# Optimization experiments

Measured on AMD Instinct MI355X. Metric: run time of the kernel, lower is better.

The kernel has to match this reference:

```python
import jax, jax.numpy as jnp
import numpy as np

B, S, D, H = 16, 512, 256, 8
DH = D // H


def setup_inputs() -> dict:
    key = jax.random.key(0)
    ks = jax.random.split(key, 10)
    w_scale = 1.0 / np.sqrt(D)
    query = jax.random.normal(ks[0], (B, S, D), dtype=jnp.float32)
    key_t = jax.random.normal(ks[1], (B, S, D), dtype=jnp.float32)
    value = jax.random.normal(ks[2], (B, S, D), dtype=jnp.float32)
    rel = jax.random.uniform(ks[3], (B, S, S), dtype=jnp.float32)
    timestamp = jax.random.uniform(ks[4], (B, S, S), dtype=jnp.float32) * 100.0
    # causal mask: True = masked (future), as used by masked_fill in the torch code
    mask = jnp.broadcast_to(jnp.triu(jnp.ones((S, S), dtype=bool), k=1), (B, S, S))
    l1 = jnp.array(0.3, dtype=jnp.float32)
    l2 = jnp.array(0.4, dtype=jnp.float32)
    Wq = jax.random.normal(ks[5], (D, D), dtype=jnp.float32) * w_scale
    Wk = jax.random.normal(ks[6], (D, D), dtype=jnp.float32) * w_scale
    Wv = jax.random.normal(ks[7], (D, D), dtype=jnp.float32) * w_scale
    bq = jnp.zeros((D,), dtype=jnp.float32)
    bk = jnp.zeros((D,), dtype=jnp.float32)
    bv = jnp.zeros((D,), dtype=jnp.float32)
    return {"query": query, "key": key_t, "value": value, "rel": rel,
            "timestamp": timestamp, "mask": mask, "l1": l1, "l2": l2,
            "Wq": Wq, "bq": bq, "Wk": Wk, "bk": bk, "Wv": Wv, "bv": bv}


def _proj(x, W, b):
    # nn.Linear: x @ W.T + b, then split heads -> [B, H, S, DH]
    return (x @ W.T + b).reshape(B, S, H, DH).transpose(0, 2, 1, 3)


def reference(query, key, value, rel, timestamp, mask, l1, l2,
              Wq, bq, Wk, bk, Wv, bv):
    q = _proj(query, Wq, bq)
    k = _proj(key, Wk, bk)
    v = _proj(value, Wv, bv)
    m = mask[:, None]                      # [B,1,S,S], broadcasts over heads
    # relative-coefficient attention: keep rel where mask True, -10000 elsewhere
    relf = rel[:, None] * m.astype(jnp.float32)
    rel_attn = jax.nn.softmax(jnp.where(relf == 0, jnp.float32(-10000.0), relf), axis=-1)
    # scaled dot-product scores
    scores = jnp.einsum('bhqd,bhkd->bhqk', q, k) / jnp.sqrt(jnp.float32(DH))
    scores = jnp.where(m, jnp.float32(-1e9), scores)
    # time-decay attention
    ts = jnp.exp(-jnp.abs(timestamp))[:, None]
    ts = jnp.where(m, -jnp.inf, ts)
    prob_attn = jax.nn.softmax(scores, axis=-1)
    time_attn = jax.nn.softmax(ts, axis=-1)
    prob_attn = (1 - l2) * prob_attn + l2 * time_attn
    prob_attn = (1 - l1) * prob_attn + l1 * rel_attn
    out = jnp.einsum('bhqk,bhkd->bhqd', prob_attn, v)
    out = out.transpose(0, 2, 1, 3).reshape(B, S, D)
    return out, prob_attn
```

## Files before the change

kernel.cpp:

```cpp
#include <hip/hip_runtime.h>
#include <hip/hip_bf16.h>

static constexpr int cB  = 16;
static constexpr int cS  = 512;
static constexpr int cD  = 256;
static constexpr int cH  = 8;
static constexpr int cDH = 32;
static constexpr size_t cNE = (size_t)cB * cS * cD;

typedef __attribute__((ext_vector_type(8))) short short8v;
typedef __attribute__((ext_vector_type(4))) short short4v;
typedef __attribute__((ext_vector_type(4))) float f32x4;

__device__ __forceinline__ short bfbits(float x) {
    __hip_bfloat16 h = __float2bfloat16(x);
    short s; __builtin_memcpy(&s, &h, 2); return s;
}
__device__ __forceinline__ float bff(short s) {
    __hip_bfloat16 h; __builtin_memcpy(&h, &s, 2); return __bfloat162float(h);
}

__global__ __launch_bounds__(256) void proj_kernel(
    const float* __restrict__ q_in, const float* __restrict__ k_in,
    const float* __restrict__ v_in,
    const float* __restrict__ Wq, const float* __restrict__ bq,
    const float* __restrict__ Wk, const float* __restrict__ bk,
    const float* __restrict__ Wv, const float* __restrict__ bv,
    float* __restrict__ ws)
{
    const int z = blockIdx.y;
    const float* X    = (z == 0) ? q_in : (z == 1) ? k_in : v_in;
    const float* W    = (z == 0) ? Wq   : (z == 1) ? Wk   : Wv;
    const float* bias = (z == 0) ? bq   : (z == 1) ? bk   : bv;
    short* HI  = (short*)ws + (size_t)z * 2 * cNE;
    short* LO  = HI + cNE;
    short* VTb = (short*)(ws + 2 * cNE);

    const int tid  = threadIdx.x;
    const int w    = tid >> 6;
    const int lane = tid & 63;
    const int n16  = lane & 15;
    const int quad = lane >> 4;

    const int i0 = blockIdx.x * 32 + 16 * (w & 1);
    const int j0 = 128 * (w >> 1);

    const float* xrow = X + (size_t)(i0 + n16) * cD + quad * 8;
    short8v a_hi[8], a_lo[8];
#pragma unroll
    for (int c = 0; c < 8; c++) {
        float xa[8];
        *(float4*)&xa[0] = *(const float4*)(xrow + c * 32);
        *(float4*)&xa[4] = *(const float4*)(xrow + c * 32 + 4);
#pragma unroll
        for (int j = 0; j < 8; j++) {
            short hb = bfbits(xa[j]);
            a_hi[c][j] = hb;
            a_lo[c][j] = bfbits(xa[j] - bff(hb));
        }
    }

#pragma unroll
    for (int t = 0; t < 8; t++) {
        const int jb = j0 + t * 16;
        const float* wrow = W + (size_t)(jb + n16) * cD + quad * 8;
        f32x4 acc = (f32x4){0.f, 0.f, 0.f, 0.f};
#pragma unroll
        for (int c = 0; c < 8; c++) {
            float wv_[8];
            *(float4*)&wv_[0] = *(const float4*)(wrow + c * 32);
            *(float4*)&wv_[4] = *(const float4*)(wrow + c * 32 + 4);
            short8v b_hi, b_lo;
#pragma unroll
            for (int j = 0; j < 8; j++) {
                short hb = bfbits(wv_[j]);
                b_hi[j] = hb;
                b_lo[j] = bfbits(wv_[j] - bff(hb));
            }
            acc = __builtin_amdgcn_mfma_f32_16x16x32_bf16(a_hi[c], b_hi, acc, 0, 0, 0);
            acc = __builtin_amdgcn_mfma_f32_16x16x32_bf16(a_hi[c], b_lo, acc, 0, 0, 0);
            acc = __builtin_amdgcn_mfma_f32_16x16x32_bf16(a_lo[c], b_hi, acc, 0, 0, 0);
        }
        const int jg = jb + n16;
        const float bv_ = bias[jg];
        const int h_ = jg >> 5, dh = jg & 31;
        if (z == 2) {
#pragma unroll
            for (int r = 0; r < 4; r++) {
                int gi = i0 + quad * 4 + r;
                int b_ = gi >> 9, s_ = gi & 511;
                VTb[(((size_t)(b_ * cH + h_)) * cDH + dh) * cS + s_] =
                    bfbits(acc[r] + bv_);
            }
        } else {
#pragma unroll
            for (int r = 0; r < 4; r++) {
                int gi = i0 + quad * 4 + r;
                int b_ = gi >> 9, s_ = gi & 511;
                size_t idx = (((size_t)(b_ * cH + h_)) * cS + s_) * cDH + dh;
                float v = acc[r] + bv_;
                short hb2 = bfbits(v);
                HI[idx] = hb2;
                LO[idx] = bfbits(v - bff(hb2));
            }
        }
    }
}

__global__ __launch_bounds__(256) void ev_kernel(
    const float* __restrict__ rel, const float* __restrict__ ts,
    const float* __restrict__ l1p, const float* __restrict__ l2p,
    short* __restrict__ Evb)
{
    const int w = threadIdx.x >> 6, lane = threadIdx.x & 63;
    const int row = blockIdx.x * 4 + w;
    const int q = row & 511;
    const float* tr = ts  + (size_t)row * cS;
    const float* rr = rel + (size_t)row * cS;
    const float l1 = l1p[0], l2 = l2p[0];
    const float Bc = (1.f - l1) * l2;
    const float Cc = l1;

    float tv[8], rv[8];
    float tmax = -1e30f, rmax = -1e30f;
#pragma unroll
    for (int j = 0; j < 8; j++) {
        int k = lane + 64 * j;
        float tl_ = (k <= q) ? tr[k] : 0.f;
        float r   = (k >  q) ? rr[k] : 0.f;
        tv[j] = (k <= q) ? __expf(-fabsf(tl_)) : -1e30f;
        rv[j] = (k > q && r != 0.f) ? r : -10000.f;
        tmax = fmaxf(tmax, tv[j]);
        rmax = fmaxf(rmax, rv[j]);
    }
#pragma unroll
    for (int m = 1; m < 64; m <<= 1) {
        tmax = fmaxf(tmax, __shfl_xor(tmax, m, 64));
        rmax = fmaxf(rmax, __shfl_xor(rmax, m, 64));
    }
    float te[8], re[8];
    float tsum = 0.f, rsum = 0.f;
#pragma unroll
    for (int j = 0; j < 8; j++) {
        te[j] = (tv[j] > -1e29f) ? __expf(tv[j] - tmax) : 0.f;
        re[j] = __expf(rv[j] - rmax);
        tsum += te[j]; rsum += re[j];
    }
#pragma unroll
    for (int m = 1; m < 64; m <<= 1) {
        tsum += __shfl_xor(tsum, m, 64);
        rsum += __shfl_xor(rsum, m, 64);
    }
    const float ti = Bc / tsum, ri = Cc / rsum;
#pragma unroll
    for (int j = 0; j < 8; j++) {
        int k = lane + 64 * j;
        Evb[(size_t)row * cS + k] = bfbits(te[j] * ti + re[j] * ri);
    }
}

__global__ __launch_bounds__(256, 4) void attn2_kernel(
    const float* __restrict__ ws, const short* __restrict__ Evb,
    const float* __restrict__ l1p, const float* __restrict__ l2p,
    float* __restrict__ out, float* __restrict__ prob)
{
    constexpr int PS = 536;
    __shared__ short Pl[32 * PS];
    __shared__ float redM[2][32];
    __shared__ float redS[2][32];

    const int tid  = threadIdx.x;
    const int w    = tid >> 6;
    const int lane = tid & 63;
    const int n16  = lane & 15;
    const int quad = lane >> 4;

    const int flat = blockIdx.y * gridDim.x + blockIdx.x;
    const int xcd  = flat & 7;
    const int slot = flat >> 3;
    const int b  = xcd + 8 * (slot >> 7);
    const int h  = (slot >> 4) & 7;
    const int qt = slot & 15;
    const size_t bh = (size_t)b * cH + h;
    const int q0 = qt * 32;

    const short* Qhi = (const short*)ws;
    const short* Qlo = Qhi + cNE;
    const short* Khi = Qhi + 2 * cNE;
    const short* Klo = Qhi + 3 * cNE;
    const short* VTb = (const short*)(ws + 2 * cNE);

    const float l1 = l1p[0], l2 = l2p[0];
    const float Ac = (1.f - l1) * (1.f - l2);

    const int qhH = w & 1;
    const int kh2 = w >> 1;
    const int kbase = 256 * kh2;

    const int rowA = q0 + 16 * qhH + n16;
    const size_t qoff = (bh * cS + rowA) * cDH + quad * 8;
    short8v a_hi = *(const short8v*)(Qhi + qoff);
    short8v a_lo = *(const short8v*)(Qlo + qoff);

    const int tl = (kbase <= q0 + 31) ? min(15, (q0 + 31 - kbase) >> 4) : -1;
    f32x4 acc[16];
#pragma unroll
    for (int t = 0; t < 16; t++) {
        acc[t] = (f32x4){0.f, 0.f, 0.f, 0.f};
        if (t <= tl) {
            const size_t koff = (bh * cS + kbase + 16 * t + n16) * cDH + quad * 8;
            short8v b_hi = *(const short8v*)(Khi + koff);
            short8v b_lo = *(const short8v*)(Klo + koff);
            acc[t] = __builtin_amdgcn_mfma_f32_16x16x32_bf16(a_hi, b_hi, acc[t], 0, 0, 0);
            acc[t] = __builtin_amdgcn_mfma_f32_16x16x32_bf16(a_hi, b_lo, acc[t], 0, 0, 0);
            acc[t] = __builtin_amdgcn_mfma_f32_16x16x32_bf16(a_lo, b_hi, acc[t], 0, 0, 0);
        }
    }

    const float scale = 0.17677669529663687f;
    const int rowDl = 16 * qhH + quad * 4;
    float Mx0 = -1e30f, Mx1 = -1e30f, Mx2 = -1e30f, Mx3 = -1e30f;
#pragma unroll
    for (int t = 0; t < 16; t++) {
        const int kg = kbase + 16 * t + n16;
        const int rg = q0 + rowDl;
        float s0 = (kg <= rg + 0) ? acc[t][0] * scale : -1e30f;
        float s1 = (kg <= rg + 1) ? acc[t][1] * scale : -1e30f;
        float s2 = (kg <= rg + 2) ? acc[t][2] * scale : -1e30f;
        float s3 = (kg <= rg + 3) ? acc[t][3] * scale : -1e30f;
        acc[t][0] = s0; acc[t][1] = s1; acc[t][2] = s2; acc[t][3] = s3;
        Mx0 = fmaxf(Mx0, s0); Mx1 = fmaxf(Mx1, s1);
        Mx2 = fmaxf(Mx2, s2); Mx3 = fmaxf(Mx3, s3);
    }
#pragma unroll
    for (int m = 1; m < 16; m <<= 1) {
        Mx0 = fmaxf(Mx0, __shfl_xor(Mx0, m, 64));
        Mx1 = fmaxf(Mx1, __shfl_xor(Mx1, m, 64));
        Mx2 = fmaxf(Mx2, __shfl_xor(Mx2, m, 64));
        Mx3 = fmaxf(Mx3, __shfl_xor(Mx3, m, 64));
    }
    if (n16 == 0) {
        redM[kh2][rowDl + 0] = Mx0; redM[kh2][rowDl + 1] = Mx1;
        redM[kh2][rowDl + 2] = Mx2; redM[kh2][rowDl + 3] = Mx3;
    }
    __syncthreads();
    float Mg0 = fmaxf(redM[0][rowDl + 0], redM[1][rowDl + 0]);
    float Mg1 = fmaxf(redM[0][rowDl + 1], redM[1][rowDl + 1]);
    float Mg2 = fmaxf(redM[0][rowDl + 2], redM[1][rowDl + 2]);
    float Mg3 = fmaxf(redM[0][rowDl + 3], redM[1][rowDl + 3]);

    float S0 = 0.f, S1 = 0.f, S2 = 0.f, S3 = 0.f;
#pragma unroll
    for (int t = 0; t < 16; t++) {
        float e0 = __expf(acc[t][0] - Mg0);
        float e1 = __expf(acc[t][1] - Mg1);
        float e2 = __expf(acc[t][2] - Mg2);
        float e3 = __expf(acc[t][3] - Mg3);
        acc[t][0] = e0; acc[t][1] = e1; acc[t][2] = e2; acc[t][3] = e3;
        S0 += e0; S1 += e1; S2 += e2; S3 += e3;
    }
#pragma unroll
    for (int m = 1; m < 16; m <<= 1) {
        S0 += __shfl_xor(S0, m, 64); S1 += __shfl_xor(S1, m, 64);
        S2 += __shfl_xor(S2, m, 64); S3 += __shfl_xor(S3, m, 64);
    }
    if (n16 == 0) {
        redS[kh2][rowDl + 0] = S0; redS[kh2][rowDl + 1] = S1;
        redS[kh2][rowDl + 2] = S2; redS[kh2][rowDl + 3] = S3;
    }
    __syncthreads();
    const float i0 = Ac / (redS[0][rowDl + 0] + redS[1][rowDl + 0]);
    const float i1 = Ac / (redS[0][rowDl + 1] + redS[1][rowDl + 1]);
    const float i2 = Ac / (redS[0][rowDl + 2] + redS[1][rowDl + 2]);
    const float i3 = Ac / (redS[0][rowDl + 3] + redS[1][rowDl + 3]);

#pragma unroll
    for (int t = 0; t < 16; t++) {
        const int col = kbase + 16 * t + n16;
        Pl[(rowDl + 0) * PS + col] = bfbits(acc[t][0] * i0);
        Pl[(rowDl + 1) * PS + col] = bfbits(acc[t][1] * i1);
        Pl[(rowDl + 2) * PS + col] = bfbits(acc[t][2] * i2);
        Pl[(rowDl + 3) * PS + col] = bfbits(acc[t][3] * i3);
    }
    __syncthreads();

#pragma unroll
    for (int it = 0; it < 16; it++) {
        const int idx = it * 256 + tid;
        const int r = idx >> 7;
        const int c0 = (idx & 127) * 4;
        short* pp = &Pl[r * PS + c0];
        short4v pv = *(short4v*)pp;
        const short4v ev = *(const short4v*)(Evb + ((size_t)(b * cS + q0 + r)) * cS + c0);
        f32x4 o;
#pragma unroll
        for (int j = 0; j < 4; j++) o[j] = bff(pv[j]) + bff(ev[j]);
        __builtin_nontemporal_store(o, (f32x4*)(prob + (bh * cS + q0 + r) * cS + c0));
#pragma unroll
        for (int j = 0; j < 4; j++) pv[j] = bfbits(o[j]);
        *(short4v*)pp = pv;
    }
    __syncthreads();

    const int dhT = w & 1, qT = w >> 1;
    const int dhA = 16 * dhT + n16;
    const short* vtrow = VTb + (bh * cDH + dhA) * cS;
    f32x4 oacc = (f32x4){0.f, 0.f, 0.f, 0.f};
#pragma unroll
    for (int k0 = 0; k0 < cS; k0 += 32) {
        short8v av = *(const short8v*)(vtrow + k0 + quad * 8);
        short8v bv = *(short8v*)&Pl[(16 * qT + n16) * PS + k0 + quad * 8];
        oacc = __builtin_amdgcn_mfma_f32_16x16x32_bf16(av, bv, oacc, 0, 0, 0);
    }
    const int qg = q0 + 16 * qT + n16;
    const int dhD = 16 * dhT + quad * 4;
    float* op = out + ((size_t)b * cS + qg) * cD + h * cDH + dhD;
    __builtin_nontemporal_store(oacc, (f32x4*)op);
}

extern "C" void kernel_launch(void* const* d_in, const int* in_sizes, int n_in,
                              void* d_out, int out_size, void* d_ws, size_t ws_size,
                              hipStream_t stream) {
    const float* query = (const float*)d_in[0];
    const float* key   = (const float*)d_in[1];
    const float* value = (const float*)d_in[2];
    const float* rel   = (const float*)d_in[3];
    const float* tsp   = (const float*)d_in[4];
    const float* l1 = (const float*)d_in[6];
    const float* l2 = (const float*)d_in[7];
    const float* Wq = (const float*)d_in[8];
    const float* bq = (const float*)d_in[9];
    const float* Wk = (const float*)d_in[10];
    const float* bk = (const float*)d_in[11];
    const float* Wv = (const float*)d_in[12];
    const float* bv = (const float*)d_in[13];

    float* ws   = (float*)d_ws;
    short* Evb  = (short*)(ws + 3 * cNE);
    float* out  = (float*)d_out;
    float* prob = out + cNE;

    proj_kernel<<<dim3(256, 3), 256, 0, stream>>>(query, key, value,
                                                  Wq, bq, Wk, bk, Wv, bv, ws);
    ev_kernel<<<dim3(2048), 256, 0, stream>>>(rel, tsp, l1, l2, Evb);
    attn2_kernel<<<dim3(16, 128), 256, 0, stream>>>(ws, Evb, l1, l2, out, prob);
}
```

Before: 289.4 us.

## Pre-split weights to bf16 hi/lo once and fuse projection with mixing-prep kernel

```diff
diff --git a/kernel.cpp b/kernel.cpp
--- a/kernel.cpp
+++ b/kernel.cpp
@@ -7,6 +7,7 @@
 static constexpr int cH  = 8;
 static constexpr int cDH = 32;
 static constexpr size_t cNE = (size_t)cB * cS * cD;
+static constexpr size_t cWN = (size_t)cD * cD;
 
 typedef __attribute__((ext_vector_type(8))) short short8v;
 typedef __attribute__((ext_vector_type(4))) short short4v;
@@ -20,142 +21,155 @@
     __hip_bfloat16 h; __builtin_memcpy(&h, &s, 2); return __bfloat162float(h);
 }
 
-__global__ __launch_bounds__(256) void proj_kernel(
-    const float* __restrict__ q_in, const float* __restrict__ k_in,
-    const float* __restrict__ v_in,
-    const float* __restrict__ Wq, const float* __restrict__ bq,
-    const float* __restrict__ Wk, const float* __restrict__ bk,
-    const float* __restrict__ Wv, const float* __restrict__ bv,
-    float* __restrict__ ws)
+__global__ __launch_bounds__(256) void wsplit_kernel(
+    const float* __restrict__ Wq, const float* __restrict__ Wk,
+    const float* __restrict__ Wv, short* __restrict__ Wsp)
 {
     const int z = blockIdx.y;
-    const float* X    = (z == 0) ? q_in : (z == 1) ? k_in : v_in;
-    const float* W    = (z == 0) ? Wq   : (z == 1) ? Wk   : Wv;
-    const float* bias = (z == 0) ? bq   : (z == 1) ? bk   : bv;
-    short* HI  = (short*)ws + (size_t)z * 2 * cNE;
-    short* LO  = HI + cNE;
-    short* VTb = (short*)(ws + 2 * cNE);
-
-    const int tid  = threadIdx.x;
+    const float* W = (z == 0) ? Wq : (z == 1) ? Wk : Wv;
+    short* hi = Wsp + (size_t)z * 2 * cWN;
+    short* lo = hi + cWN;
+    const int i = (blockIdx.x * 256 + threadIdx.x) * 4;
+    float4 v = *(const float4*)(W + i);
+    float va[4] = {v.x, v.y, v.z, v.w};
+    short4v h, l;
+#pragma unroll
+    for (int j = 0; j < 4; j++) {
+        short hb = bfbits(va[j]);
+        h[j] = hb;
+        l[j] = bfbits(va[j] - bff(hb));
+    }
+    *(short4v*)(hi + i) = h;
+    *(short4v*)(lo + i) = l;
+}
+
+__global__ __launch_bounds__(256) void prep_kernel(
+    const float* __restrict__ q_in, const float* __restrict__ k_in,
+    const float* __restrict__ v_in, const short* __restrict__ Wsp,
+    const float* __restrict__ bq, const float* __restrict__ bk,
+    const float* __restrict__ bv,
+    const float* __restrict__ rel, const float* __restrict__ ts,
+    const float* __restrict__ l1p, const float* __restrict__ l2p,
+    float* __restrict__ ws, short* __restrict__ Evb)
+{
+    const int bid = blockIdx.x;
+    const int tid = threadIdx.x;
     const int w    = tid >> 6;
     const int lane = tid & 63;
-    const int n16  = lane & 15;
-    const int quad = lane >> 4;
-
-    const int i0 = blockIdx.x * 32 + 16 * (w & 1);
-    const int j0 = 128 * (w >> 1);
-
-    const float* xrow = X + (size_t)(i0 + n16) * cD + quad * 8;
-    short8v a_hi[8], a_lo[8];
-#pragma unroll
-    for (int c = 0; c < 8; c++) {
-        float xa[8];
-        *(float4*)&xa[0] = *(const float4*)(xrow + c * 32);
-        *(float4*)&xa[4] = *(const float4*)(xrow + c * 32 + 4);
+
+    if (bid < 768) {
+        const int z  = bid >> 8;
+        const int bx = bid & 255;
+        const float* X    = (z == 0) ? q_in : (z == 1) ? k_in : v_in;
+        const float* bias = (z == 0) ? bq   : (z == 1) ? bk   : bv;
+        const short* Whi = Wsp + (size_t)z * 2 * cWN;
+        const short* Wlo = Whi + cWN;
+        short* HI  = (short*)ws + (size_t)z * 2 * cNE;
+        short* LO  = HI + cNE;
+        short* VTb = (short*)(ws + 2 * cNE);
+
+        const int n16  = lane & 15;
+        const int quad = lane >> 4;
+        const int i0 = bx * 32 + 16 * (w & 1);
+        const int j0 = 128 * (w >> 1);
+
+        const float* xrow = X + (size_t)(i0 + n16) * cD + quad * 8;
+        short8v a_hi[8], a_lo[8];
+#pragma unroll
+        for (int c = 0; c < 8; c++) {
+            float xa[8];
+            *(float4*)&xa[0] = *(const float4*)(xrow + c * 32);
+            *(float4*)&xa[4] = *(const float4*)(xrow + c * 32 + 4);
+#pragma unroll
+            for (int j = 0; j < 8; j++) {
+                short hb = bfbits(xa[j]);
+                a_hi[c][j] = hb;
+                a_lo[c][j] = bfbits(xa[j] - bff(hb));
+            }
+        }
+
+#pragma unroll
+        for (int t = 0; t < 8; t++) {
+            const int jb = j0 + t * 16;
+            const size_t wbase = (size_t)(jb + n16) * cD + quad * 8;
+            f32x4 acc = (f32x4){0.f, 0.f, 0.f, 0.f};
+#pragma unroll
+            for (int c = 0; c < 8; c++) {
+                short8v b_hi = *(const short8v*)(Whi + wbase + c * 32);
+                short8v b_lo = *(const short8v*)(Wlo + wbase + c * 32);
+                acc = __builtin_amdgcn_mfma_f32_16x16x32_bf16(a_hi[c], b_hi, acc, 0, 0, 0);
+                acc = __builtin_amdgcn_mfma_f32_16x16x32_bf16(a_hi[c], b_lo, acc, 0, 0, 0);
+                acc = __builtin_amdgcn_mfma_f32_16x16x32_bf16(a_lo[c], b_hi, acc, 0, 0, 0);
+            }
+            const int jg = jb + n16;
+            const float bv_ = bias[jg];
+            const int h_ = jg >> 5, dh = jg & 31;
+            if (z == 2) {
+#pragma unroll
+                for (int r = 0; r < 4; r++) {
+                    int gi = i0 + quad * 4 + r;
+                    int b_ = gi >> 9, s_ = gi & 511;
+                    VTb[(((size_t)(b_ * cH + h_)) * cDH + dh) * cS + s_] =
+                        bfbits(acc[r] + bv_);
+                }
+            } else {
+#pragma unroll
+                for (int r = 0; r < 4; r++) {
+                    int gi = i0 + quad * 4 + r;
+                    int b_ = gi >> 9, s_ = gi & 511;
+                    size_t idx = (((size_t)(b_ * cH + h_)) * cS + s_) * cDH + dh;
+                    float v = acc[r] + bv_;
+                    short hb2 = bfbits(v);
+                    HI[idx] = hb2;
+                    LO[idx] = bfbits(v - bff(hb2));
+                }
+            }
+        }
+    } else {
+        const int row = (bid - 768) * 4 + w;
+        const int q = row & 511;
+        const float* tr = ts  + (size_t)row * cS;
+        const float* rr = rel + (size_t)row * cS;
+        const float l1 = l1p[0], l2 = l2p[0];
+        const float Bc = (1.f - l1) * l2;
+        const float Cc = l1;
+
+        float tv[8], rv[8];
+        float tmax = -1e30f, rmax = -1e30f;
 #pragma unroll
         for (int j = 0; j < 8; j++) {
-            short hb = bfbits(xa[j]);
-            a_hi[c][j] = hb;
-            a_lo[c][j] = bfbits(xa[j] - bff(hb));
-        }
-    }
-
-#pragma unroll
-    for (int t = 0; t < 8; t++) {
-        const int jb = j0 + t * 16;
-        const float* wrow = W + (size_t)(jb + n16) * cD + quad * 8;
-        f32x4 acc = (f32x4){0.f, 0.f, 0.f, 0.f};
-#pragma unroll
-        for (int c = 0; c < 8; c++) {
-            float wv_[8];
-            *(float4*)&wv_[0] = *(const float4*)(wrow + c * 32);
-            *(float4*)&wv_[4] = *(const float4*)(wrow + c * 32 + 4);
-            short8v b_hi, b_lo;
-#pragma unroll
-            for (int j = 0; j < 8; j++) {
-                short hb = bfbits(wv_[j]);
-                b_hi[j] = hb;
-                b_lo[j] = bfbits(wv_[j] - bff(hb));
-            }
-            acc = __builtin_amdgcn_mfma_f32_16x16x32_bf16(a_hi[c], b_hi, acc, 0, 0, 0);
-            acc = __builtin_amdgcn_mfma_f32_16x16x32_bf16(a_hi[c], b_lo, acc, 0, 0, 0);
-            acc = __builtin_amdgcn_mfma_f32_16x16x32_bf16(a_lo[c], b_hi, acc, 0, 0, 0);
-        }
-        const int jg = jb + n16;
-        const float bv_ = bias[jg];
-        const int h_ = jg >> 5, dh = jg & 31;
-        if (z == 2) {
-#pragma unroll
-            for (int r = 0; r < 4; r++) {
-                int gi = i0 + quad * 4 + r;
-                int b_ = gi >> 9, s_ = gi & 511;
-                VTb[(((size_t)(b_ * cH + h_)) * cDH + dh) * cS + s_] =
-                    bfbits(acc[r] + bv_);
-            }
-        } else {
-#pragma unroll
-            for (int r = 0; r < 4; r++) {
-                int gi = i0 + quad * 4 + r;
-                int b_ = gi >> 9, s_ = gi & 511;
-                size_t idx = (((size_t)(b_ * cH + h_)) * cS + s_) * cDH + dh;
-                float v = acc[r] + bv_;
-                short hb2 = bfbits(v);
-                HI[idx] = hb2;
-                LO[idx] = bfbits(v - bff(hb2));
-            }
-        }
-    }
-}
-
-__global__ __launch_bounds__(256) void ev_kernel(
-    const float* __restrict__ rel, const float* __restrict__ ts,
-    const float* __restrict__ l1p, const float* __restrict__ l2p,
-    short* __restrict__ Evb)
-{
-    const int w = threadIdx.x >> 6, lane = threadIdx.x & 63;
-    const int row = blockIdx.x * 4 + w;
-    const int q = row & 511;
-    const float* tr = ts  + (size_t)row * cS;
-    const float* rr = rel + (size_t)row * cS;
-    const float l1 = l1p[0], l2 = l2p[0];
-    const float Bc = (1.f - l1) * l2;
-    const float Cc = l1;
-
-    float tv[8], rv[8];
-    float tmax = -1e30f, rmax = -1e30f;
-#pragma unroll
-    for (int j = 0; j < 8; j++) {
-        int k = lane + 64 * j;
-        float tl_ = (k <= q) ? tr[k] : 0.f;
-        float r   = (k >  q) ? rr[k] : 0.f;
-        tv[j] = (k <= q) ? __expf(-fabsf(tl_)) : -1e30f;
-        rv[j] = (k > q && r != 0.f) ? r : -10000.f;
-        tmax = fmaxf(tmax, tv[j]);
-        rmax = fmaxf(rmax, rv[j]);
-    }
-#pragma unroll
-    for (int m = 1; m < 64; m <<= 1) {
-        tmax = fmaxf(tmax, __shfl_xor(tmax, m, 64));
-        rmax = fmaxf(rmax, __shfl_xor(rmax, m, 64));
-    }
-    float te[8], re[8];
-    float tsum = 0.f, rsum = 0.f;
-#pragma unroll
-    for (int j = 0; j < 8; j++) {
-        te[j] = (tv[j] > -1e29f) ? __expf(tv[j] - tmax) : 0.f;
-        re[j] = __expf(rv[j] - rmax);
-        tsum += te[j]; rsum += re[j];
-    }
-#pragma unroll
-    for (int m = 1; m < 64; m <<= 1) {
-        tsum += __shfl_xor(tsum, m, 64);
-        rsum += __shfl_xor(rsum, m, 64);
-    }
-    const float ti = Bc / tsum, ri = Cc / rsum;
-#pragma unroll
-    for (int j = 0; j < 8; j++) {
-        int k = lane + 64 * j;
-        Evb[(size_t)row * cS + k] = bfbits(te[j] * ti + re[j] * ri);
+            int k = lane + 64 * j;
+            float tl_ = (k <= q) ? tr[k] : 0.f;
+            float r   = (k >  q) ? rr[k] : 0.f;
+            tv[j] = (k <= q) ? __expf(-fabsf(tl_)) : -1e30f;
+            rv[j] = (k > q && r != 0.f) ? r : -10000.f;
+            tmax = fmaxf(tmax, tv[j]);
+            rmax = fmaxf(rmax, rv[j]);
+        }
+#pragma unroll
+        for (int m = 1; m < 64; m <<= 1) {
+            tmax = fmaxf(tmax, __shfl_xor(tmax, m, 64));
+            rmax = fmaxf(rmax, __shfl_xor(rmax, m, 64));
+        }
+        float te[8], re[8];
+        float tsum = 0.f, rsum = 0.f;
+#pragma unroll
+        for (int j = 0; j < 8; j++) {
+            te[j] = (tv[j] > -1e29f) ? __expf(tv[j] - tmax) : 0.f;
+            re[j] = __expf(rv[j] - rmax);
+            tsum += te[j]; rsum += re[j];
+        }
+#pragma unroll
+        for (int m = 1; m < 64; m <<= 1) {
+            tsum += __shfl_xor(tsum, m, 64);
+            rsum += __shfl_xor(rsum, m, 64);
+        }
+        const float ti = Bc / tsum, ri = Cc / rsum;
+#pragma unroll
+        for (int j = 0; j < 8; j++) {
+            int k = lane + 64 * j;
+            Evb[(size_t)row * cS + k] = bfbits(te[j] * ti + re[j] * ri);
+        }
     }
 }
 
@@ -337,11 +351,13 @@
 
     float* ws   = (float*)d_ws;
     short* Evb  = (short*)(ws + 3 * cNE);
+    short* Wsp  = Evb + (size_t)cB * cS * cS;
     float* out  = (float*)d_out;
     float* prob = out + cNE;
 
-    proj_kernel<<<dim3(256, 3), 256, 0, stream>>>(query, key, value,
-                                                  Wq, bq, Wk, bk, Wv, bv, ws);
-    ev_kernel<<<dim3(2048), 256, 0, stream>>>(rel, tsp, l1, l2, Evb);
+    wsplit_kernel<<<dim3(64, 3), 256, 0, stream>>>(Wq, Wk, Wv, Wsp);
+    prep_kernel<<<dim3(2816), 256, 0, stream>>>(query, key, value, Wsp,
+                                                bq, bk, bv, rel, tsp,
+                                                l1, l2, ws, Evb);
     attn2_kernel<<<dim3(16, 128), 256, 0, stream>>>(ws, Evb, l1, l2, out, prob);
 }
```

Result: faster. 283.2 us (-2.1%).
